# Kernel optimization log

Hardware: AMD Instinct MI355X
Metric: run time of the kernel (lower is better)

Reference implementation:

```python
import jax, jax.numpy as jnp
import numpy as np

B = 131072
W = {'center': 0.2, 'diag': 0.15, 'quat': 0.15, 'canonical': 0.1, 'corner': 0.2, 'iou': 0.2}

# 8 corner sign combinations of a unit box, projection planes (xz, xy, yz) and perpendicular axes
_SIGNS = np.array([[sx, sy, sz] for sx in (1., -1.) for sy in (1., -1.) for sz in (1., -1.)], np.float32)
_PLANES = np.array([[0, 2], [0, 1], [1, 2]])
_PERP = np.array([1, 2, 0])


def quat_to_mat(q):
    # q: (..., 4) in [x, y, z, w] order -> (..., 3, 3)
    x, y, z, w = q[..., 0], q[..., 1], q[..., 2], q[..., 3]
    m = jnp.stack([1 - 2*y*y - 2*z*z, 2*x*y - 2*z*w, 2*x*z + 2*y*w,
                   2*x*y + 2*z*w, 1 - 2*x*x - 2*z*z, 2*y*z - 2*x*w,
                   2*x*z - 2*y*w, 2*y*z + 2*x*w, 1 - 2*x*x - 2*y*y], axis=-1)
    return m.reshape(q.shape[:-1] + (3, 3))


def corners_from_params(params):
    # params: (B, 10) = [center(3), dims(3), quat(4)] -> corners (B, 8, 3)
    c, d, q = params[:, :3], params[:, 3:6], params[:, 6:10]
    q = q / (jnp.linalg.norm(q, axis=-1, keepdims=True) + 1e-8)
    R = quat_to_mat(q)
    local = jnp.asarray(_SIGNS)[None, :, :] * (0.5 * d[:, None, :])  # (B,8,3)
    return c[:, None, :] + jnp.einsum('bij,bkj->bki', R, local)


def quat_loss(pq, gq):
    pq = pq / (jnp.linalg.norm(pq, axis=-1, keepdims=True) + 1e-6)
    gq = gq / (jnp.linalg.norm(gq, axis=-1, keepdims=True) + 1e-6)
    # pred_basis = pred_mat @ I = pred_mat; dots = |pred_mat^T @ gt_mat|
    dots = jnp.abs(jnp.einsum('bki,bkj->bij', quat_to_mat(pq), quat_to_mat(gq)))
    ang = jnp.arccos(jnp.clip(dots.max(-1), 1e-6, 1.0))  # max over gt axes per pred axis
    return ang.mean()


def canonical_loss(pd, gd, pq, gq, dims_weight=0.5, angular_weight=0.5):
    pq = pq / (jnp.linalg.norm(pq, axis=-1, keepdims=True) + 1e-8)
    gq = gq / (jnp.linalg.norm(gq, axis=-1, keepdims=True) + 1e-8)
    pi = jnp.argsort(-pd, axis=1)
    gi = jnp.argsort(-gd, axis=1)
    ps = jnp.take_along_axis(pd, pi, axis=1)
    gs = jnp.take_along_axis(gd, gi, axis=1)
    dims_loss = (jnp.abs(ps - gs) / (gs + 1e-8)).mean()
    # basis[perm] rows == one_hot(perm)
    P = jax.nn.one_hot(pi, 3, dtype=pd.dtype)
    G = jax.nn.one_hot(gi, 3, dtype=gd.dtype)
    pr = jnp.einsum('bij,bjk->bik', quat_to_mat(pq), P)
    gr = jnp.einsum('bij,bjk->bik', quat_to_mat(gq), G)
    abs_dots = jnp.abs(jnp.sum(pr * gr, axis=-1))  # (B,3) rowwise dots
    ang = jnp.arccos(jnp.clip(abs_dots, 0.0, 1.0))
    return dims_weight * dims_loss + angular_weight * ang.mean()


def _assignment_cost(cost):
    # Exact 8x8 linear assignment (== scipy linear_sum_assignment optimum) via
    # bitmask DP, vectorized over batch. Grad flows through the argmin path,
    # matching the gradient of the selected-assignment distances.
    dp = [None] * 256
    dp[0] = jnp.zeros(cost.shape[:1], cost.dtype)
    for mask in range(1, 256):
        r = bin(mask).count('1') - 1  # next row to assign
        cands = [dp[mask ^ (1 << j)] + cost[:, r, j] for j in range(8) if (mask >> j) & 1]
        dp[mask] = cands[0] if len(cands) == 1 else jnp.min(jnp.stack(cands, -1), -1)
    return dp[255]


def corner_distance_loss(pc, gc, gt_diag):
    # pc, gc: (B,8,3); gt_diag: (B,)
    cost = jnp.abs(pc[:, :, None, :] - gc[:, None, :, :]).sum(-1)  # (B,8,8) pairwise L1
    return _assignment_cost(cost) / 8.0 / (gt_diag + 1e-6)  # mean over 8 matched corners


def projected_iou(c1, c2, eps=1e-3):
    p1 = jnp.transpose(c1[:, :, _PLANES], (0, 2, 1, 3))  # (B,3,8,2)
    p2 = jnp.transpose(c2[:, :, _PLANES], (0, 2, 1, 3))
    min1, max1 = p1.min(2), p1.max(2)
    min2, max2 = p2.min(2), p2.max(2)
    inter = jnp.prod(jnp.clip(jnp.minimum(max1, max2) - jnp.maximum(min1, min2) + eps, 0.0, None), -1)
    a1 = jnp.prod(max1 - min1 + eps, -1)
    a2 = jnp.prod(max2 - min2 + eps, -1)
    iou2d = inter / (a1 + a2 - inter + 1e-6)
    h1min, h1max = c1[:, :, _PERP].min(1), c1[:, :, _PERP].max(1)
    h2min, h2max = c2[:, :, _PERP].min(1), c2[:, :, _PERP].max(1)
    hi = jnp.clip(jnp.minimum(h1max, h2max) - jnp.maximum(h1min, h2min), 0.0, None)
    hu = (h1max - h1min) + (h2max - h2min) - hi
    iou = iou2d * (hi / (hu + 1e-6))
    return jnp.clip(iou.mean(1), 0.0, 1.0)


def setup_inputs() -> dict:
    key = jax.random.key(0)
    k1, k2 = jax.random.split(key)
    pred_params = jax.random.uniform(k1, (B, 10), jnp.float32)
    gt_params = jax.random.uniform(k2, (B, 10), jnp.float32)
    return {"pred_params": pred_params, "gt_params": gt_params}


def reference(pred_params, gt_params):
    gt_dims = gt_params[:, 3:6]
    gt_diag = jnp.linalg.norm(gt_dims, axis=-1)  # (B,)
    total = W['diag'] * (jnp.abs(pred_params[:, 3:6] - gt_dims) / (gt_dims + 1e-6)).mean()
    total = total + W['center'] * (jnp.abs(pred_params[:, :3] - gt_params[:, :3]) / gt_diag[:, None]).mean()
    total = total + W['quat'] * quat_loss(pred_params[:, 6:], gt_params[:, 6:])
    total = total + W['canonical'] * canonical_loss(pred_params[:, 3:6], gt_dims,
                                                    pred_params[:, 6:], gt_params[:, 6:])
    pc = corners_from_params(pred_params)
    gc = corners_from_params(gt_params)
    total = total + W['corner'] * corner_distance_loss(pc, gc, gt_diag).mean()
    total = total + W['iou'] * (1.0 - projected_iou(pc, gc).mean())
    return total
```

## Files before the change

kernel.cpp:

```cpp
#include <hip/hip_runtime.h>
#include <math.h>

#define BLOCK 256

template <int I> struct IC { static constexpr int value = I; };

template <int I, int N, typename F>
__device__ __forceinline__ void static_for(F&& f) {
  if constexpr (I < N) {
    f(IC<I>{});
    static_for<I + 1, N>(f);
  }
}

constexpr int permute_bits(int k, int p) {
  int b2 = (k >> 2) & 1, b1 = (k >> 1) & 1, b0 = k & 1;
  switch (p) {
    case 0: return (b2 << 2) | (b1 << 1) | b0;
    case 1: return (b2 << 2) | (b0 << 1) | b1;
    case 2: return (b1 << 2) | (b2 << 1) | b0;
    case 3: return (b1 << 2) | (b0 << 1) | b2;
    case 4: return (b0 << 2) | (b2 << 1) | b1;
    default: return (b0 << 2) | (b1 << 1) | b2;
  }
}

__device__ __forceinline__ float acos_fast(float x) {
  float r = sqrtf(fmaxf(1.0f - x, 0.0f));
  float p = fmaf(x, -0.0187293f, 0.0742610f);
  p = fmaf(x, p, -0.2121144f);
  p = fmaf(x, p, 1.5707288f);
  return r * p;
}

__device__ __forceinline__ void quat_mat(float x, float y, float z, float w,
                                         float eps, float R[9]) {
  float n = sqrtf(x * x + y * y + z * z + w * w);
  float s = 1.0f / (n + eps);
  x *= s; y *= s; z *= s; w *= s;
  R[0] = 1.0f - 2.0f * y * y - 2.0f * z * z;
  R[1] = 2.0f * x * y - 2.0f * z * w;
  R[2] = 2.0f * x * z + 2.0f * y * w;
  R[3] = 2.0f * x * y + 2.0f * z * w;
  R[4] = 1.0f - 2.0f * x * x - 2.0f * z * z;
  R[5] = 2.0f * y * z - 2.0f * x * w;
  R[6] = 2.0f * x * z - 2.0f * y * w;
  R[7] = 2.0f * y * z + 2.0f * x * w;
  R[8] = 1.0f - 2.0f * x * x - 2.0f * y * y;
}

__device__ __forceinline__ float sel3(float v0, float v1, float v2, int i) {
  return i == 0 ? v0 : (i == 1 ? v1 : v2);
}
__device__ __forceinline__ int sel3i(int v0, int v1, int v2, int i) {
  return i == 0 ? v0 : (i == 1 ? v1 : v2);
}

__global__ __launch_bounds__(BLOCK)
void hybrid_loss_kernel(const float* __restrict__ pred,
                        const float* __restrict__ gt,
                        float* __restrict__ out, int B, float invB) {
  int b = blockIdx.x * BLOCK + threadIdx.x;
  float contrib = 0.0f;
  if (b < B) {
    const float2* p2 = reinterpret_cast<const float2*>(pred) + (size_t)b * 5;
    const float2* g2 = reinterpret_cast<const float2*>(gt) + (size_t)b * 5;
    float2 pA = p2[0], pB = p2[1], pC = p2[2], pD = p2[3], pE = p2[4];
    float2 gA = g2[0], gB = g2[1], gC = g2[2], gD = g2[3], gE = g2[4];
    float px = pA.x, py = pA.y, pz = pB.x;
    float pdx = pB.y, pdy = pC.x, pdz = pC.y;
    float pqx = pD.x, pqy = pD.y, pqz = pE.x, pqw = pE.y;
    float gx = gA.x, gy = gA.y, gz = gB.x;
    float gdx = gB.y, gdy = gC.x, gdz = gC.y;
    float gqx = gD.x, gqy = gD.y, gqz = gE.x, gqw = gE.y;

    float gdiag = sqrtf(gdx * gdx + gdy * gdy + gdz * gdz);
    float corner_scale = 0.2f * 0.125f / (gdiag + 1e-6f);

    float s_diag = fabsf(pdx - gdx) / (gdx + 1e-6f)
                 + fabsf(pdy - gdy) / (gdy + 1e-6f)
                 + fabsf(pdz - gdz) / (gdz + 1e-6f);
    float s_center = (fabsf(px - gx) + fabsf(py - gy) + fabsf(pz - gz)) / gdiag;

    float Rp[9], Rg[9];
    quat_mat(pqx, pqy, pqz, pqw, 1e-8f, Rp);
    quat_mat(gqx, gqy, gqz, gqw, 1e-8f, Rg);

    float s_quat = 0.0f;
#pragma unroll
    for (int i = 0; i < 3; ++i) {
      float m = 0.0f;
#pragma unroll
      for (int j = 0; j < 3; ++j) {
        float d = fabsf(Rp[i] * Rg[j] + Rp[3 + i] * Rg[3 + j] +
                        Rp[6 + i] * Rg[6 + j]);
        m = fmaxf(m, d);
      }
      m = fminf(fmaxf(m, 1e-6f), 1.0f);
      s_quat += acos_fast(m);
    }

    int q0 = 0, q1 = 1, q2 = 2;
    float v0 = pdx, v1 = pdy, v2 = pdz;
    if (v1 > v0) { float t = v0; v0 = v1; v1 = t; int ti = q0; q0 = q1; q1 = ti; }
    if (v2 > v1) { float t = v1; v1 = v2; v2 = t; int ti = q1; q1 = q2; q2 = ti; }
    if (v1 > v0) { float t = v0; v0 = v1; v1 = t; int ti = q0; q0 = q1; q1 = ti; }
    int r0 = 0, r1 = 1, r2 = 2;
    float u0 = gdx, u1 = gdy, u2 = gdz;
    if (u1 > u0) { float t = u0; u0 = u1; u1 = t; int ti = r0; r0 = r1; r1 = ti; }
    if (u2 > u1) { float t = u1; u1 = u2; u2 = t; int ti = r1; r1 = r2; r2 = ti; }
    if (u1 > u0) { float t = u0; u0 = u1; u1 = t; int ti = r0; r0 = r1; r1 = ti; }

    float s_cdims = fabsf(v0 - u0) / (u0 + 1e-8f)
                  + fabsf(v1 - u1) / (u1 + 1e-8f)
                  + fabsf(v2 - u2) / (u2 + 1e-8f);

    int ig0 = (r0 == 0) ? 0 : ((r1 == 0) ? 1 : 2);
    int ig1 = (r0 == 1) ? 0 : ((r1 == 1) ? 1 : 2);
    int ig2 = (r0 == 2) ? 0 : ((r1 == 2) ? 1 : 2);
    int t0 = sel3i(ig0, ig1, ig2, q0);
    int t1 = sel3i(ig0, ig1, ig2, q1);
    int t2 = sel3i(ig0, ig1, ig2, q2);

    float s_cang = 0.0f;
#pragma unroll
    for (int i = 0; i < 3; ++i) {
      float gg0 = Rg[i * 3 + 0], gg1 = Rg[i * 3 + 1], gg2 = Rg[i * 3 + 2];
      float ds = Rp[i * 3 + 0] * sel3(gg0, gg1, gg2, t0)
               + Rp[i * 3 + 1] * sel3(gg0, gg1, gg2, t1)
               + Rp[i * 3 + 2] * sel3(gg0, gg1, gg2, t2);
      float ad = fminf(fabsf(ds), 1.0f);
      s_cang += acos_fast(ad);
    }

    float phx = 0.5f * pdx, phy = 0.5f * pdy, phz = 0.5f * pdz;
    float ghx = 0.5f * gdx, ghy = 0.5f * gdy, ghz = 0.5f * gdz;
    float pA0x = Rp[0] * phx, pA0y = Rp[3] * phx, pA0z = Rp[6] * phx;
    float pA1x = Rp[1] * phy, pA1y = Rp[4] * phy, pA1z = Rp[7] * phy;
    float pA2x = Rp[2] * phz, pA2y = Rp[5] * phz, pA2z = Rp[8] * phz;
    float gA0x = Rg[0] * ghx, gA0y = Rg[3] * ghx, gA0z = Rg[6] * ghx;
    float gA1x = Rg[1] * ghy, gA1y = Rg[4] * ghy, gA1z = Rg[7] * ghy;
    float gA2x = Rg[2] * ghz, gA2y = Rg[5] * ghz, gA2z = Rg[8] * ghz;

    float pcx[8], pcy[8], pcz[8], gcx[8], gcy[8], gcz[8];
#pragma unroll
    for (int k = 0; k < 8; ++k) {
      float sx = (k & 4) ? -1.0f : 1.0f;
      float sy = (k & 2) ? -1.0f : 1.0f;
      float sz = (k & 1) ? -1.0f : 1.0f;
      pcx[k] = px + sx * pA0x + sy * pA1x + sz * pA2x;
      pcy[k] = py + sx * pA0y + sy * pA1y + sz * pA2y;
      pcz[k] = pz + sx * pA0z + sy * pA1z + sz * pA2z;
      gcx[k] = gx + sx * gA0x + sy * gA1x + sz * gA2x;
      gcy[k] = gy + sx * gA0y + sy * gA1y + sz * gA2y;
      gcz[k] = gz + sx * gA0z + sy * gA1z + sz * gA2z;
    }

    float pmnx = pcx[0], pmxx = pcx[0], pmny = pcy[0], pmxy = pcy[0];
    float pmnz = pcz[0], pmxz = pcz[0];
    float gmnx = gcx[0], gmxx = gcx[0], gmny = gcy[0], gmxy = gcy[0];
    float gmnz = gcz[0], gmxz = gcz[0];
#pragma unroll
    for (int k = 1; k < 8; ++k) {
      pmnx = fminf(pmnx, pcx[k]); pmxx = fmaxf(pmxx, pcx[k]);
      pmny = fminf(pmny, pcy[k]); pmxy = fmaxf(pmxy, pcy[k]);
      pmnz = fminf(pmnz, pcz[k]); pmxz = fmaxf(pmxz, pcz[k]);
      gmnx = fminf(gmnx, gcx[k]); gmxx = fmaxf(gmxx, gcx[k]);
      gmny = fminf(gmny, gcy[k]); gmxy = fmaxf(gmxy, gcy[k]);
      gmnz = fminf(gmnz, gcz[k]); gmxz = fmaxf(gmxz, gcz[k]);
    }

    auto plane_iou = [&](float a1n, float a1x, float b1n, float b1x,
                         float a2n, float a2x, float b2n, float b2x,
                         float p1n, float p1x, float p2n, float p2x) -> float {
      const float eps = 1e-3f;
      float ia = fmaxf(fminf(a1x, a2x) - fmaxf(a1n, a2n) + eps, 0.0f);
      float ib = fmaxf(fminf(b1x, b2x) - fmaxf(b1n, b2n) + eps, 0.0f);
      float inter = ia * ib;
      float ar1 = (a1x - a1n + eps) * (b1x - b1n + eps);
      float ar2 = (a2x - a2n + eps) * (b2x - b2n + eps);
      float iou2d = inter / (ar1 + ar2 - inter + 1e-6f);
      float hi = fmaxf(fminf(p1x, p2x) - fmaxf(p1n, p2n), 0.0f);
      float hu = (p1x - p1n) + (p2x - p2n) - hi;
      return iou2d * (hi / (hu + 1e-6f));
    };
    float iou_sum = 0.0f;
    iou_sum += plane_iou(pmnx, pmxx, pmnz, pmxz, gmnx, gmxx, gmnz, gmxz,
                         pmny, pmxy, gmny, gmxy);
    iou_sum += plane_iou(pmnx, pmxx, pmny, pmxy, gmnx, gmxx, gmny, gmxy,
                         pmnz, pmxz, gmnz, gmxz);
    iou_sum += plane_iou(pmny, pmxy, pmnz, pmxz, gmny, gmxy, gmnz, gmxz,
                         pmnx, pmxx, gmnx, gmxx);
    float iou_b = fminf(fmaxf(iou_sum * (1.0f / 3.0f), 0.0f), 1.0f);

    float D[8][8];
#pragma unroll
    for (int r = 0; r < 8; ++r)
#pragma unroll
      for (int j = 0; j < 8; ++j)
        D[r][j] = fabsf(pcx[r] - gcx[j]) + fabsf(pcy[r] - gcy[j]) +
                  fabsf(pcz[r] - gcz[j]);

    float best = 3.0e38f;
    static_for<0, 48>([&](auto A) {
      constexpr int p = decltype(A)::value / 8;
      constexpr int m = decltype(A)::value & 7;
      float sum = D[0][permute_bits(0, p) ^ m];
      static_for<1, 8>([&](auto K) {
        constexpr int k = decltype(K)::value;
        sum += D[k][permute_bits(k, p) ^ m];
      });
      best = fminf(best, sum);
    });

    const float third = (1.0f / 3.0f);
    float loss_b = 0.15f * s_diag * third
                 + 0.2f * s_center * third
                 + 0.15f * s_quat * third
                 + 0.1f * (0.5f * s_cdims * third + 0.5f * s_cang * third)
                 + best * corner_scale
                 - 0.2f * iou_b;
    contrib = loss_b * invB;
    if (b == 0) contrib += 0.2f;
  }

  float s = contrib;
#pragma unroll
  for (int off = 32; off > 0; off >>= 1) s += __shfl_down(s, off, 64);
  __shared__ float red[BLOCK / 64];
  int lane = threadIdx.x & 63;
  int wid = threadIdx.x >> 6;
  if (lane == 0) red[wid] = s;
  __syncthreads();
  if (threadIdx.x == 0) {
    float tot = red[0] + red[1] + red[2] + red[3];
    atomicAdd(out, tot);
  }
}

extern "C" void kernel_launch(void* const* d_in, const int* in_sizes, int n_in,
                              void* d_out, int out_size, void* d_ws, size_t ws_size,
                              hipStream_t stream) {
  const float* pred = (const float*)d_in[0];
  const float* gt = (const float*)d_in[1];
  float* out = (float*)d_out;
  int B = in_sizes[0] / 10;
  hipMemsetAsync(out, 0, sizeof(float), stream);
  int grid = (B + BLOCK - 1) / BLOCK;
  hybrid_loss_kernel<<<grid, BLOCK, 0, stream>>>(pred, gt, out, B,
                                                 1.0f / (float)B);
}
```

Measured before the change: 69.92 us.

## Split per-box work across two wave roles and compute AABB extents analytically

Each block now handles 128 boxes using 256 threads. Two waves compute the diag, center, quat, canonical and IoU terms, while the other two waves compute the corners and the 48-permutation corner-matching minimum for the same boxes. The IoU axis-aligned bounds are now derived analytically from the absolute rotated half-axes instead of a min/max over the 8 corners. This doubles the thread count and separates branch-free code paths per wave, which should lower register pressure and raise parallelism. The cost is duplicated input loads and rotation-matrix construction in both roles.

```diff
diff --git a/kernel.cpp b/kernel.cpp
--- a/kernel.cpp
+++ b/kernel.cpp
@@ -60,8 +60,12 @@
 void hybrid_loss_kernel(const float* __restrict__ pred,
                         const float* __restrict__ gt,
                         float* __restrict__ out, int B, float invB) {
-  int b = blockIdx.x * BLOCK + threadIdx.x;
+  int lane = threadIdx.x & 63;
+  int wid = threadIdx.x >> 6;
+  int role = wid >> 1;
+  int b = blockIdx.x * 128 + (wid & 1) * 64 + lane;
   float contrib = 0.0f;
+
   if (b < B) {
     const float2* p2 = reinterpret_cast<const float2*>(pred) + (size_t)b * 5;
     const float2* g2 = reinterpret_cast<const float2*>(gt) + (size_t)b * 5;
@@ -75,63 +79,10 @@
     float gqx = gD.x, gqy = gD.y, gqz = gE.x, gqw = gE.y;
 
     float gdiag = sqrtf(gdx * gdx + gdy * gdy + gdz * gdz);
-    float corner_scale = 0.2f * 0.125f / (gdiag + 1e-6f);
-
-    float s_diag = fabsf(pdx - gdx) / (gdx + 1e-6f)
-                 + fabsf(pdy - gdy) / (gdy + 1e-6f)
-                 + fabsf(pdz - gdz) / (gdz + 1e-6f);
-    float s_center = (fabsf(px - gx) + fabsf(py - gy) + fabsf(pz - gz)) / gdiag;
 
     float Rp[9], Rg[9];
     quat_mat(pqx, pqy, pqz, pqw, 1e-8f, Rp);
     quat_mat(gqx, gqy, gqz, gqw, 1e-8f, Rg);
-
-    float s_quat = 0.0f;
-#pragma unroll
-    for (int i = 0; i < 3; ++i) {
-      float m = 0.0f;
-#pragma unroll
-      for (int j = 0; j < 3; ++j) {
-        float d = fabsf(Rp[i] * Rg[j] + Rp[3 + i] * Rg[3 + j] +
-                        Rp[6 + i] * Rg[6 + j]);
-        m = fmaxf(m, d);
-      }
-      m = fminf(fmaxf(m, 1e-6f), 1.0f);
-      s_quat += acos_fast(m);
-    }
-
-    int q0 = 0, q1 = 1, q2 = 2;
-    float v0 = pdx, v1 = pdy, v2 = pdz;
-    if (v1 > v0) { float t = v0; v0 = v1; v1 = t; int ti = q0; q0 = q1; q1 = ti; }
-    if (v2 > v1) { float t = v1; v1 = v2; v2 = t; int ti = q1; q1 = q2; q2 = ti; }
-    if (v1 > v0) { float t = v0; v0 = v1; v1 = t; int ti = q0; q0 = q1; q1 = ti; }
-    int r0 = 0, r1 = 1, r2 = 2;
-    float u0 = gdx, u1 = gdy, u2 = gdz;
-    if (u1 > u0) { float t = u0; u0 = u1; u1 = t; int ti = r0; r0 = r1; r1 = ti; }
-    if (u2 > u1) { float t = u1; u1 = u2; u2 = t; int ti = r1; r1 = r2; r2 = ti; }
-    if (u1 > u0) { float t = u0; u0 = u1; u1 = t; int ti = r0; r0 = r1; r1 = ti; }
-
-    float s_cdims = fabsf(v0 - u0) / (u0 + 1e-8f)
-                  + fabsf(v1 - u1) / (u1 + 1e-8f)
-                  + fabsf(v2 - u2) / (u2 + 1e-8f);
-
-    int ig0 = (r0 == 0) ? 0 : ((r1 == 0) ? 1 : 2);
-    int ig1 = (r0 == 1) ? 0 : ((r1 == 1) ? 1 : 2);
-    int ig2 = (r0 == 2) ? 0 : ((r1 == 2) ? 1 : 2);
-    int t0 = sel3i(ig0, ig1, ig2, q0);
-    int t1 = sel3i(ig0, ig1, ig2, q1);
-    int t2 = sel3i(ig0, ig1, ig2, q2);
-
-    float s_cang = 0.0f;
-#pragma unroll
-    for (int i = 0; i < 3; ++i) {
-      float gg0 = Rg[i * 3 + 0], gg1 = Rg[i * 3 + 1], gg2 = Rg[i * 3 + 2];
-      float ds = Rp[i * 3 + 0] * sel3(gg0, gg1, gg2, t0)
-               + Rp[i * 3 + 1] * sel3(gg0, gg1, gg2, t1)
-               + Rp[i * 3 + 2] * sel3(gg0, gg1, gg2, t2);
-      float ad = fminf(fabsf(ds), 1.0f);
-      s_cang += acos_fast(ad);
-    }
 
     float phx = 0.5f * pdx, phy = 0.5f * pdy, phz = 0.5f * pdz;
     float ghx = 0.5f * gdx, ghy = 0.5f * gdy, ghz = 0.5f * gdz;
@@ -142,95 +93,153 @@
     float gA1x = Rg[1] * ghy, gA1y = Rg[4] * ghy, gA1z = Rg[7] * ghy;
     float gA2x = Rg[2] * ghz, gA2y = Rg[5] * ghz, gA2z = Rg[8] * ghz;
 
-    float pcx[8], pcy[8], pcz[8], gcx[8], gcy[8], gcz[8];
-#pragma unroll
-    for (int k = 0; k < 8; ++k) {
-      float sx = (k & 4) ? -1.0f : 1.0f;
-      float sy = (k & 2) ? -1.0f : 1.0f;
-      float sz = (k & 1) ? -1.0f : 1.0f;
-      pcx[k] = px + sx * pA0x + sy * pA1x + sz * pA2x;
-      pcy[k] = py + sx * pA0y + sy * pA1y + sz * pA2y;
-      pcz[k] = pz + sx * pA0z + sy * pA1z + sz * pA2z;
-      gcx[k] = gx + sx * gA0x + sy * gA1x + sz * gA2x;
-      gcy[k] = gy + sx * gA0y + sy * gA1y + sz * gA2y;
-      gcz[k] = gz + sx * gA0z + sy * gA1z + sz * gA2z;
+    if (role == 0) {
+      float s_diag = fabsf(pdx - gdx) / (gdx + 1e-6f)
+                   + fabsf(pdy - gdy) / (gdy + 1e-6f)
+                   + fabsf(pdz - gdz) / (gdz + 1e-6f);
+      float s_center =
+          (fabsf(px - gx) + fabsf(py - gy) + fabsf(pz - gz)) / gdiag;
+
+      float s_quat = 0.0f;
+#pragma unroll
+      for (int i = 0; i < 3; ++i) {
+        float m = 0.0f;
+#pragma unroll
+        for (int j = 0; j < 3; ++j) {
+          float d = fabsf(Rp[i] * Rg[j] + Rp[3 + i] * Rg[3 + j] +
+                          Rp[6 + i] * Rg[6 + j]);
+          m = fmaxf(m, d);
+        }
+        m = fminf(fmaxf(m, 1e-6f), 1.0f);
+        s_quat += acos_fast(m);
+      }
+
+      int q0 = 0, q1 = 1, q2 = 2;
+      float v0 = pdx, v1 = pdy, v2 = pdz;
+      if (v1 > v0) { float t = v0; v0 = v1; v1 = t; int ti = q0; q0 = q1; q1 = ti; }
+      if (v2 > v1) { float t = v1; v1 = v2; v2 = t; int ti = q1; q1 = q2; q2 = ti; }
+      if (v1 > v0) { float t = v0; v0 = v1; v1 = t; int ti = q0; q0 = q1; q1 = ti; }
+      int r0 = 0, r1 = 1, r2 = 2;
+      float u0 = gdx, u1 = gdy, u2 = gdz;
+      if (u1 > u0) { float t = u0; u0 = u1; u1 = t; int ti = r0; r0 = r1; r1 = ti; }
+      if (u2 > u1) { float t = u1; u1 = u2; u2 = t; int ti = r1; r1 = r2; r2 = ti; }
+      if (u1 > u0) { float t = u0; u0 = u1; u1 = t; int ti = r0; r0 = r1; r1 = ti; }
+
+      float s_cdims = fabsf(v0 - u0) / (u0 + 1e-8f)
+                    + fabsf(v1 - u1) / (u1 + 1e-8f)
+                    + fabsf(v2 - u2) / (u2 + 1e-8f);
+
+      int ig0 = (r0 == 0) ? 0 : ((r1 == 0) ? 1 : 2);
+      int ig1 = (r0 == 1) ? 0 : ((r1 == 1) ? 1 : 2);
+      int ig2 = (r0 == 2) ? 0 : ((r1 == 2) ? 1 : 2);
+      int t0 = sel3i(ig0, ig1, ig2, q0);
+      int t1 = sel3i(ig0, ig1, ig2, q1);
+      int t2 = sel3i(ig0, ig1, ig2, q2);
+
+      float s_cang = 0.0f;
+#pragma unroll
+      for (int i = 0; i < 3; ++i) {
+        float gg0 = Rg[i * 3 + 0], gg1 = Rg[i * 3 + 1], gg2 = Rg[i * 3 + 2];
+        float ds = Rp[i * 3 + 0] * sel3(gg0, gg1, gg2, t0)
+                 + Rp[i * 3 + 1] * sel3(gg0, gg1, gg2, t1)
+                 + Rp[i * 3 + 2] * sel3(gg0, gg1, gg2, t2);
+        float ad = fminf(fabsf(ds), 1.0f);
+        s_cang += acos_fast(ad);
+      }
+
+      float pex = fabsf(pA0x) + fabsf(pA1x) + fabsf(pA2x);
+      float pey = fabsf(pA0y) + fabsf(pA1y) + fabsf(pA2y);
+      float pez = fabsf(pA0z) + fabsf(pA1z) + fabsf(pA2z);
+      float gex = fabsf(gA0x) + fabsf(gA1x) + fabsf(gA2x);
+      float gey = fabsf(gA0y) + fabsf(gA1y) + fabsf(gA2y);
+      float gez = fabsf(gA0z) + fabsf(gA1z) + fabsf(gA2z);
+      float pmnx = px - pex, pmxx = px + pex;
+      float pmny = py - pey, pmxy = py + pey;
+      float pmnz = pz - pez, pmxz = pz + pez;
+      float gmnx = gx - gex, gmxx = gx + gex;
+      float gmny = gy - gey, gmxy = gy + gey;
+      float gmnz = gz - gez, gmxz = gz + gez;
+
+      auto plane_iou = [&](float a1n, float a1x, float b1n, float b1x,
+                           float a2n, float a2x, float b2n, float b2x,
+                           float p1n, float p1x, float p2n,
+                           float p2x) -> float {
+        const float eps = 1e-3f;
+        float ia = fmaxf(fminf(a1x, a2x) - fmaxf(a1n, a2n) + eps, 0.0f);
+        float ib = fmaxf(fminf(b1x, b2x) - fmaxf(b1n, b2n) + eps, 0.0f);
+        float inter = ia * ib;
+        float ar1 = (a1x - a1n + eps) * (b1x - b1n + eps);
+        float ar2 = (a2x - a2n + eps) * (b2x - b2n + eps);
+        float iou2d = inter / (ar1 + ar2 - inter + 1e-6f);
+        float hi = fmaxf(fminf(p1x, p2x) - fmaxf(p1n, p2n), 0.0f);
+        float hu = (p1x - p1n) + (p2x - p2n) - hi;
+        return iou2d * (hi / (hu + 1e-6f));
+      };
+      float iou_sum = 0.0f;
+      iou_sum += plane_iou(pmnx, pmxx, pmnz, pmxz, gmnx, gmxx, gmnz, gmxz,
+                           pmny, pmxy, gmny, gmxy);
+      iou_sum += plane_iou(pmnx, pmxx, pmny, pmxy, gmnx, gmxx, gmny, gmxy,
+                           pmnz, pmxz, gmnz, gmxz);
+      iou_sum += plane_iou(pmny, pmxy, pmnz, pmxz, gmny, gmxy, gmnz, gmxz,
+                           pmnx, pmxx, gmnx, gmxx);
+      float iou_b = fminf(fmaxf(iou_sum * (1.0f / 3.0f), 0.0f), 1.0f);
+
+      const float third = (1.0f / 3.0f);
+      float loss_a = 0.15f * s_diag * third
+                   + 0.2f * s_center * third
+                   + 0.15f * s_quat * third
+                   + 0.1f * (0.5f * s_cdims * third + 0.5f * s_cang * third)
+                   - 0.2f * iou_b;
+      contrib = loss_a * invB;
+      if (b == 0) contrib += 0.2f;
+    } else {
+      float corner_scale = 0.2f * 0.125f / (gdiag + 1e-6f);
+
+      float pcx[8], pcy[8], pcz[8], gcx[8], gcy[8], gcz[8];
+#pragma unroll
+      for (int k = 0; k < 8; ++k) {
+        float sx = (k & 4) ? -1.0f : 1.0f;
+        float sy = (k & 2) ? -1.0f : 1.0f;
+        float sz = (k & 1) ? -1.0f : 1.0f;
+        pcx[k] = px + sx * pA0x + sy * pA1x + sz * pA2x;
+        pcy[k] = py + sx * pA0y + sy * pA1y + sz * pA2y;
+        pcz[k] = pz + sx * pA0z + sy * pA1z + sz * pA2z;
+        gcx[k] = gx + sx * gA0x + sy * gA1x + sz * gA2x;
+        gcy[k] = gy + sx * gA0y + sy * gA1y + sz * gA2y;
+        gcz[k] = gz + sx * gA0z + sy * gA1z + sz * gA2z;
+      }
+
+      float D[8][8];
+#pragma unroll
+      for (int r = 0; r < 8; ++r)
+#pragma unroll
+        for (int j = 0; j < 8; ++j)
+          D[r][j] = fabsf(pcx[r] - gcx[j]) + fabsf(pcy[r] - gcy[j]) +
+                    fabsf(pcz[r] - gcz[j]);
+
+      float best = 3.0e38f;
+      static_for<0, 48>([&](auto A) {
+        constexpr int p = decltype(A)::value / 8;
+        constexpr int m = decltype(A)::value & 7;
+        float sum = D[0][permute_bits(0, p) ^ m];
+        static_for<1, 8>([&](auto K) {
+          constexpr int k = decltype(K)::value;
+          sum += D[k][permute_bits(k, p) ^ m];
+        });
+        best = fminf(best, sum);
+      });
+
+      contrib = best * corner_scale * invB;
     }
-
-    float pmnx = pcx[0], pmxx = pcx[0], pmny = pcy[0], pmxy = pcy[0];
-    float pmnz = pcz[0], pmxz = pcz[0];
-    float gmnx = gcx[0], gmxx = gcx[0], gmny = gcy[0], gmxy = gcy[0];
-    float gmnz = gcz[0], gmxz = gcz[0];
-#pragma unroll
-    for (int k = 1; k < 8; ++k) {
-      pmnx = fminf(pmnx, pcx[k]); pmxx = fmaxf(pmxx, pcx[k]);
-      pmny = fminf(pmny, pcy[k]); pmxy = fmaxf(pmxy, pcy[k]);
-      pmnz = fminf(pmnz, pcz[k]); pmxz = fmaxf(pmxz, pcz[k]);
-      gmnx = fminf(gmnx, gcx[k]); gmxx = fmaxf(gmxx, gcx[k]);
-      gmny = fminf(gmny, gcy[k]); gmxy = fmaxf(gmxy, gcy[k]);
-      gmnz = fminf(gmnz, gcz[k]); gmxz = fmaxf(gmxz, gcz[k]);
-    }
-
-    auto plane_iou = [&](float a1n, float a1x, float b1n, float b1x,
-                         float a2n, float a2x, float b2n, float b2x,
-                         float p1n, float p1x, float p2n, float p2x) -> float {
-      const float eps = 1e-3f;
-      float ia = fmaxf(fminf(a1x, a2x) - fmaxf(a1n, a2n) + eps, 0.0f);
-      float ib = fmaxf(fminf(b1x, b2x) - fmaxf(b1n, b2n) + eps, 0.0f);
-      float inter = ia * ib;
-      float ar1 = (a1x - a1n + eps) * (b1x - b1n + eps);
-      float ar2 = (a2x - a2n + eps) * (b2x - b2n + eps);
-      float iou2d = inter / (ar1 + ar2 - inter + 1e-6f);
-      float hi = fmaxf(fminf(p1x, p2x) - fmaxf(p1n, p2n), 0.0f);
-      float hu = (p1x - p1n) + (p2x - p2n) - hi;
-      return iou2d * (hi / (hu + 1e-6f));
-    };
-    float iou_sum = 0.0f;
-    iou_sum += plane_iou(pmnx, pmxx, pmnz, pmxz, gmnx, gmxx, gmnz, gmxz,
-                         pmny, pmxy, gmny, gmxy);
-    iou_sum += plane_iou(pmnx, pmxx, pmny, pmxy, gmnx, gmxx, gmny, gmxy,
-                         pmnz, pmxz, gmnz, gmxz);
-    iou_sum += plane_iou(pmny, pmxy, pmnz, pmxz, gmny, gmxy, gmnz, gmxz,
-                         pmnx, pmxx, gmnx, gmxx);
-    float iou_b = fminf(fmaxf(iou_sum * (1.0f / 3.0f), 0.0f), 1.0f);
-
-    float D[8][8];
-#pragma unroll
-    for (int r = 0; r < 8; ++r)
-#pragma unroll
-      for (int j = 0; j < 8; ++j)
-        D[r][j] = fabsf(pcx[r] - gcx[j]) + fabsf(pcy[r] - gcy[j]) +
-                  fabsf(pcz[r] - gcz[j]);
-
-    float best = 3.0e38f;
-    static_for<0, 48>([&](auto A) {
-      constexpr int p = decltype(A)::value / 8;
-      constexpr int m = decltype(A)::value & 7;
-      float sum = D[0][permute_bits(0, p) ^ m];
-      static_for<1, 8>([&](auto K) {
-        constexpr int k = decltype(K)::value;
-        sum += D[k][permute_bits(k, p) ^ m];
-      });
-      best = fminf(best, sum);
-    });
-
-    const float third = (1.0f / 3.0f);
-    float loss_b = 0.15f * s_diag * third
-                 + 0.2f * s_center * third
-                 + 0.15f * s_quat * third
-                 + 0.1f * (0.5f * s_cdims * third + 0.5f * s_cang * third)
-                 + best * corner_scale
-                 - 0.2f * iou_b;
-    contrib = loss_b * invB;
-    if (b == 0) contrib += 0.2f;
   }
 
   float s = contrib;
 #pragma unroll
   for (int off = 32; off > 0; off >>= 1) s += __shfl_down(s, off, 64);
   __shared__ float red[BLOCK / 64];
-  int lane = threadIdx.x & 63;
-  int wid = threadIdx.x >> 6;
-  if (lane == 0) red[wid] = s;
+  int rlane = threadIdx.x & 63;
+  int rwid = threadIdx.x >> 6;
+  if (rlane == 0) red[rwid] = s;
   __syncthreads();
   if (threadIdx.x == 0) {
     float tot = red[0] + red[1] + red[2] + red[3];
@@ -246,7 +255,7 @@
   float* out = (float*)d_out;
   int B = in_sizes[0] / 10;
   hipMemsetAsync(out, 0, sizeof(float), stream);
-  int grid = (B + BLOCK - 1) / BLOCK;
+  int grid = (B + 127) / 128;
   hybrid_loss_kernel<<<grid, BLOCK, 0, stream>>>(pred, gt, out, B,
                                                  1.0f / (float)B);
 }
```

Result: slower. 74.53 us (+6.6%).
